# Kernel optimization log

Hardware: AMD Instinct MI355X
Metric: run time of the kernel (lower is better)

The kernel has to match this reference:

```python
import jax, jax.numpy as jnp
import numpy as np

D_MODEL = 2048
D_FF = 8192


def _act_quant(x):
    # BitNet b1.58 per-token int8 absmax activation quantization with STE passthrough
    scale = 127.0 / jnp.clip(jnp.max(jnp.abs(x), axis=-1, keepdims=True), 1e-5)
    xq = jnp.clip(jnp.round(x * scale), -128.0, 127.0) / scale
    return x + jax.lax.stop_gradient(xq - x)


def _weight_quant(w):
    # Ternary {-1,0,1} weight quantization with per-tensor mean-abs scale
    scale = 1.0 / jnp.clip(jnp.mean(jnp.abs(w)), 1e-5)
    wq = jnp.clip(jnp.round(w * scale), -1.0, 1.0) / scale
    return w + jax.lax.stop_gradient(wq - w)


def _bitlinear(x, w):
    # y = Q_act(x) @ Q_w(w)^T   (w has shape [out, in], torch Linear convention)
    return jnp.einsum('bsd,fd->bsf', _act_quant(x), _weight_quant(w))


def setup_inputs() -> dict:
    key = jax.random.key(0)
    k_x, k_w1, k_w2 = jax.random.split(key, 3)
    x = jax.random.normal(k_x, (4, 4096, D_MODEL), dtype=jnp.float32)
    # torch Linear default init scale ~ 1/sqrt(fan_in)
    W1 = jax.random.normal(k_w1, (D_FF, D_MODEL), dtype=jnp.float32) / np.sqrt(D_MODEL)
    W2 = jax.random.normal(k_w2, (D_MODEL, D_FF), dtype=jnp.float32) / np.sqrt(D_FF)
    return {"x": x, "W1": W1, "W2": W2}


def reference(x, W1, W2):
    h = jax.nn.silu(_bitlinear(x, W1))   # [B, S, d_ff]
    return _bitlinear(h, W2)             # [B, S, d_model]; dropout p=0 -> identity
```

## Files before the change

kernel.cpp:

```cpp
#include <hip/hip_runtime.h>
#include <hip/hip_bf16.h>
#include <cstdint>

#define DM 2048
#define DF 8192

typedef int v4i __attribute__((ext_vector_type(4)));

__device__ __forceinline__ float silu_f(float y) {
  return y * (1.0f / (1.0f + expf(-y)));
}

__device__ __forceinline__ void gload_lds16(const void* g, void* l) {
  __builtin_amdgcn_global_load_lds(
      (const __attribute__((address_space(1))) void*)g,
      (__attribute__((address_space(3))) void*)l, 16, 0, 0);
}

__global__ __launch_bounds__(256) void abs_sum_k(const float* __restrict__ w,
                                                 float* __restrict__ partial) {
  const int t = threadIdx.x;
  const float4* wp = (const float4*)w;
  const long base = (long)blockIdx.x * 4096;
  float s = 0.f;
#pragma unroll
  for (int i = 0; i < 16; ++i) {
    float4 v = wp[base + i * 256 + t];
    s += fabsf(v.x) + fabsf(v.y) + fabsf(v.z) + fabsf(v.w);
  }
#pragma unroll
  for (int d = 1; d < 64; d <<= 1) s += __shfl_xor(s, d, 64);
  __shared__ float wsum[4];
  if ((t & 63) == 0) wsum[t >> 6] = s;
  __syncthreads();
  if (t == 0) partial[blockIdx.x] = (wsum[0] + wsum[1]) + (wsum[2] + wsum[3]);
}

__global__ __launch_bounds__(256) void finalize_scales_k(const float* __restrict__ p1,
                                                         const float* __restrict__ p2,
                                                         float* __restrict__ sc) {
  const float* p = (blockIdx.x == 0) ? p1 : p2;
  const int t = threadIdx.x;
  float s = (p[t] + p[t + 256]) + (p[t + 512] + p[t + 768]);
#pragma unroll
  for (int d = 1; d < 64; d <<= 1) s += __shfl_xor(s, d, 64);
  __shared__ float wsum[4];
  if ((t & 63) == 0) wsum[t >> 6] = s;
  __syncthreads();
  if (t == 0) {
    float total = (wsum[0] + wsum[1]) + (wsum[2] + wsum[3]);
    float mean = total * (1.0f / 16777216.0f);
    float c = fmaxf(mean, 1e-5f);
    sc[blockIdx.x * 2 + 0] = 1.0f / c;
    sc[blockIdx.x * 2 + 1] = c;
  }
}

__global__ __launch_bounds__(256) void tern_quant_k(const float* __restrict__ w,
                                                    int8_t* __restrict__ wq,
                                                    const float* __restrict__ scp) {
  const float s = scp[0];
  const long i = (long)blockIdx.x * 256 + threadIdx.x;
  float4 v = ((const float4*)w)[i];
  int q0 = (int)rintf(v.x * s); q0 = q0 < -1 ? -1 : (q0 > 1 ? 1 : q0);
  int q1 = (int)rintf(v.y * s); q1 = q1 < -1 ? -1 : (q1 > 1 ? 1 : q1);
  int q2 = (int)rintf(v.z * s); q2 = q2 < -1 ? -1 : (q2 > 1 ? 1 : q2);
  int q3 = (int)rintf(v.w * s); q3 = q3 < -1 ? -1 : (q3 > 1 ? 1 : q3);
  ((int*)wq)[i] = (q0 & 255) | ((q1 & 255) << 8) | ((q2 & 255) << 16) | ((q3 & 255) << 24);
}

__global__ __launch_bounds__(256) void act_quant_x_k(const float* __restrict__ x,
                                                     int8_t* __restrict__ xq,
                                                     float* __restrict__ inv_sx) {
  const int t = threadIdx.x;
  const long row = blockIdx.x;
  const float4* xr = (const float4*)(x + row * DM);
  float4 v0 = xr[t * 2], v1 = xr[t * 2 + 1];
  float m = fmaxf(fmaxf(fmaxf(fabsf(v0.x), fabsf(v0.y)), fmaxf(fabsf(v0.z), fabsf(v0.w))),
                  fmaxf(fmaxf(fabsf(v1.x), fabsf(v1.y)), fmaxf(fabsf(v1.z), fabsf(v1.w))));
#pragma unroll
  for (int d = 1; d < 64; d <<= 1) m = fmaxf(m, __shfl_xor(m, d, 64));
  __shared__ float wm[4];
  if ((t & 63) == 0) wm[t >> 6] = m;
  __syncthreads();
  m = fmaxf(fmaxf(wm[0], wm[1]), fmaxf(wm[2], wm[3]));
  const float scale = 127.0f / fmaxf(m, 1e-5f);
  if (t == 0) inv_sx[row] = 1.0f / scale;
  float vv[8] = {v0.x, v0.y, v0.z, v0.w, v1.x, v1.y, v1.z, v1.w};
  int q[8];
#pragma unroll
  for (int j = 0; j < 8; ++j) {
    int qq = (int)rintf(vv[j] * scale);
    q[j] = qq < -128 ? -128 : (qq > 127 ? 127 : qq);
  }
  int lo = (q[0] & 255) | ((q[1] & 255) << 8) | ((q[2] & 255) << 16) | ((q[3] & 255) << 24);
  int hi = (q[4] & 255) | ((q[5] & 255) << 8) | ((q[6] & 255) << 16) | ((q[7] & 255) << 24);
  ((int2*)(xq + row * DM))[t] = make_int2(lo, hi);
}

template <int K, int N, int EPI>
__global__ __launch_bounds__(512, 2) void gemm8_i8_k(
    const int8_t* __restrict__ A, const int8_t* __restrict__ B,
    const float* __restrict__ rowInv, const float* __restrict__ invswp,
    short* __restrict__ Y16, float* __restrict__ rowmaxP,
    float* __restrict__ Out) {
  constexpr int NT = K / 128;
  constexpr int NBX = N / 256;
  __shared__ __align__(16) uint8_t lds[131072];

  const int t = threadIdx.x;
  const int wave = t >> 6;
  const int lane = t & 63;
  const int wr = wave >> 2;
  const int wc = wave & 3;
  const int l15 = lane & 15, l4 = lane >> 4;

  const int cpx = (int)gridDim.x >> 3;
  const int bid0 = blockIdx.x;
  const int bid = (bid0 & 7) * cpx + (bid0 >> 3);
  const int bx = bid % NBX, by = bid / NBX;
  const long arow0 = (long)by * 256;
  const long bcol0 = (long)bx * 256;

  const int8_t* Ablk = A + arow0 * K;
  const int8_t* Bblk = B + bcol0 * K;

  const int srow = t >> 3;
  const int scol = ((t & 7) ^ (srow & 7)) << 4;

  const int rAo = (wr * 128 + l15) * 128;
  const int rBo = (wc * 64 + l15) * 128;
  const int sw = (l15 & 7) << 4;
  const int cc0 = (l4 * 16) ^ sw;
  const int cc1 = (64 | (l4 * 16)) ^ sw;

  v4i acc[8][4] = {};
  v4i a[8][2], b[4][2];

#define STAGEHT(ht_)                                                             \
  do {                                                                           \
    const int ht = (ht_);                                                        \
    if (ht < 4 * NT) {                                                           \
      const int kts = ht >> 2, part = ht & 3;                                    \
      uint8_t* d0 = lds + ((kts & 1) << 16) + (part << 14) + (wave << 10);       \
      const int8_t* sp = (part < 2) ? Ablk : Bblk;                               \
      const int8_t* s0 =                                                         \
          sp + (long)(((part & 1) << 7) + srow) * K + ((long)kts << 7) + scol;   \
      gload_lds16(s0, d0);                                                       \
      gload_lds16(s0 + ((long)K << 6), d0 + 8192);                               \
    }                                                                            \
  } while (0)

#define BAR1()                                              \
  asm volatile("" ::: "memory");                            \
  __builtin_amdgcn_s_barrier();                             \
  asm volatile("s_waitcnt lgkmcnt(0)" ::: "memory")

#define BAR2()                                              \
  asm volatile("" ::: "memory");                            \
  __builtin_amdgcn_s_barrier()

#define MM(mi, ni)                                                                          \
  acc[mi][ni] = __builtin_amdgcn_mfma_i32_16x16x64_i8(a[mi][0], b[ni][0], acc[mi][ni], 0, 0, 0); \
  acc[mi][ni] = __builtin_amdgcn_mfma_i32_16x16x64_i8(a[mi][1], b[ni][1], acc[mi][ni], 0, 0, 0)

  STAGEHT(0); STAGEHT(1); STAGEHT(2); STAGEHT(3);
  STAGEHT(4); STAGEHT(5); STAGEHT(6);
  asm volatile("s_waitcnt vmcnt(6)" ::: "memory");
  __builtin_amdgcn_s_barrier();

  for (int kt = 0; kt < NT; ++kt) {
    const uint8_t* sA = lds + ((kt & 1) << 16);
    const uint8_t* sB = sA + 32768;

    #pragma unroll
    for (int mi = 0; mi < 4; ++mi) {
      a[mi][0] = *(const v4i*)(sA + rAo + mi * 2048 + cc0);
      a[mi][1] = *(const v4i*)(sA + rAo + mi * 2048 + cc1);
    }
    #pragma unroll
    for (int ni = 0; ni < 2; ++ni) {
      b[ni][0] = *(const v4i*)(sB + rBo + ni * 2048 + cc0);
      b[ni][1] = *(const v4i*)(sB + rBo + ni * 2048 + cc1);
    }
    STAGEHT(4 * kt + 7);
    BAR1();
    __builtin_amdgcn_s_setprio(1);
    MM(0, 0); MM(0, 1); MM(1, 0); MM(1, 1);
    MM(2, 0); MM(2, 1); MM(3, 0); MM(3, 1);
    __builtin_amdgcn_s_setprio(0);
    BAR2();

    #pragma unroll
    for (int mi = 4; mi < 8; ++mi) {
      a[mi][0] = *(const v4i*)(sA + rAo + mi * 2048 + cc0);
      a[mi][1] = *(const v4i*)(sA + rAo + mi * 2048 + cc1);
    }
    STAGEHT(4 * kt + 8);
    BAR1();
    __builtin_amdgcn_s_setprio(1);
    MM(4, 0); MM(4, 1); MM(5, 0); MM(5, 1);
    MM(6, 0); MM(6, 1); MM(7, 0); MM(7, 1);
    __builtin_amdgcn_s_setprio(0);
    BAR2();

    #pragma unroll
    for (int ni = 2; ni < 4; ++ni) {
      b[ni][0] = *(const v4i*)(sB + rBo + ni * 2048 + cc0);
      b[ni][1] = *(const v4i*)(sB + rBo + ni * 2048 + cc1);
    }
    STAGEHT(4 * kt + 9);
    BAR1();
    __builtin_amdgcn_s_setprio(1);
    MM(0, 2); MM(0, 3); MM(1, 2); MM(1, 3);
    MM(2, 2); MM(2, 3); MM(3, 2); MM(3, 3);
    __builtin_amdgcn_s_setprio(0);
    BAR2();

    STAGEHT(4 * kt + 10);
    BAR2();
    __builtin_amdgcn_s_setprio(1);
    MM(4, 2); MM(4, 3); MM(5, 2); MM(5, 3);
    MM(6, 2); MM(6, 3); MM(7, 2); MM(7, 3);
    __builtin_amdgcn_s_setprio(0);
    if (kt < NT - 2) {
      asm volatile("s_waitcnt vmcnt(6)" ::: "memory");
    } else if (kt == NT - 2) {
      asm volatile("s_waitcnt vmcnt(0)" ::: "memory");
    }
    BAR2();
  }

  const float invsw = invswp[0];
  if constexpr (EPI == 1) {
    __syncthreads();
    float* redmax = (float*)lds;
#pragma unroll
    for (int mi = 0; mi < 8; ++mi) {
#pragma unroll
      for (int r = 0; r < 4; ++r) {
        const int lrow = wr * 128 + mi * 16 + l4 * 4 + r;
        const long grow = arow0 + lrow;
        const float c1v = rowInv[grow] * invsw;
        float mx = 0.f;
#pragma unroll
        for (int ni = 0; ni < 4; ++ni) {
          int yi = acc[mi][ni][r];
          float h = silu_f((float)yi * c1v);
          mx = fmaxf(mx, fabsf(h));
          int ys = yi < -32767 ? -32767 : (yi > 32767 ? 32767 : yi);
          Y16[grow * (long)DF + bcol0 + wc * 64 + ni * 16 + l15] = (short)ys;
        }
#pragma unroll
        for (int d = 1; d < 16; d <<= 1) mx = fmaxf(mx, __shfl_xor(mx, d, 64));
        if (l15 == 0) redmax[lrow * 4 + wc] = mx;
      }
    }
    __syncthreads();
    if (t < 256) {
      float mm = fmaxf(fmaxf(redmax[t * 4], redmax[t * 4 + 1]),
                       fmaxf(redmax[t * 4 + 2], redmax[t * 4 + 3]));
      rowmaxP[(arow0 + t) * NBX + bx] = mm;
    }
  } else {
#pragma unroll
    for (int mi = 0; mi < 8; ++mi) {
#pragma unroll
      for (int r = 0; r < 4; ++r) {
        const long grow = arow0 + wr * 128 + mi * 16 + l4 * 4 + r;
        const float c2 = rowInv[grow] * invsw;
#pragma unroll
        for (int ni = 0; ni < 4; ++ni)
          Out[grow * N + bcol0 + wc * 64 + ni * 16 + l15] = (float)acc[mi][ni][r] * c2;
      }
    }
  }
#undef STAGEHT
#undef BAR1
#undef BAR2
#undef MM
}

__global__ __launch_bounds__(256) void quant_h_k(const short* __restrict__ Y16,
                                                 const float* __restrict__ rowmaxP,
                                                 const float* __restrict__ inv_sx,
                                                 const float* __restrict__ sc,
                                                 int8_t* __restrict__ hq,
                                                 float* __restrict__ inv_sh) {
  const int t = threadIdx.x;
  const long row = blockIdx.x;
  __shared__ float smax_s;
  if (t < 64) {
    float m = (t < 32) ? rowmaxP[row * 32 + t] : 0.f;
#pragma unroll
    for (int d = 1; d < 64; d <<= 1) m = fmaxf(m, __shfl_xor(m, d, 64));
    if (t == 0) smax_s = m;
  }
  __syncthreads();
  const float scale = 127.0f / fmaxf(smax_s, 1e-5f);
  if (t == 0) inv_sh[row] = 1.0f / scale;
  const float c1 = inv_sx[row] * sc[1];
  const short4* yp = (const short4*)(Y16 + row * DF);
  int* op = (int*)(hq + row * DF);
#pragma unroll
  for (int b = 0; b < 8; ++b) {
    short4 s4 = yp[b * 256 + t];
    short vals[4] = {s4.x, s4.y, s4.z, s4.w};
    int q[4];
#pragma unroll
    for (int j = 0; j < 4; ++j) {
      float h = silu_f((float)vals[j] * c1);
      int qq = (int)rintf(h * scale);
      q[j] = qq < -128 ? -128 : (qq > 127 ? 127 : qq);
    }
    op[b * 256 + t] = (q[0] & 255) | ((q[1] & 255) << 8) | ((q[2] & 255) << 16) | ((q[3] & 255) << 24);
  }
}

extern "C" void kernel_launch(void* const* d_in, const int* in_sizes, int n_in,
                              void* d_out, int out_size, void* d_ws, size_t ws_size,
                              hipStream_t stream) {
  const float* x = (const float*)d_in[0];
  const float* W1 = (const float*)d_in[1];
  const float* W2 = (const float*)d_in[2];
  float* out = (float*)d_out;

  uint8_t* w = (uint8_t*)d_ws;
  float* sc = (float*)(w + 0);
  float* p1 = (float*)(w + 256);
  float* p2 = (float*)(w + 256 + 4096);
  float* inv_sx = (float*)(w + 8448);
  float* inv_sh = (float*)(w + 8448 + 65536);
  float* rowmaxP = (float*)(w + 8448 + 131072);
  uint8_t* w1q = w + 8448 + 131072 + 4194304;
  uint8_t* w2q = w1q + 16777216;
  uint8_t* xq = w2q + 16777216;
  uint8_t* hq = xq + 33554432;
  short* y16 = (short*)(hq + 134217728);

  abs_sum_k<<<1024, 256, 0, stream>>>(W1, p1);
  abs_sum_k<<<1024, 256, 0, stream>>>(W2, p2);
  finalize_scales_k<<<2, 256, 0, stream>>>(p1, p2, sc);
  tern_quant_k<<<16384, 256, 0, stream>>>(W1, (int8_t*)w1q, sc + 0);
  tern_quant_k<<<16384, 256, 0, stream>>>(W2, (int8_t*)w2q, sc + 2);
  act_quant_x_k<<<16384, 256, 0, stream>>>(x, (int8_t*)xq, inv_sx);
  gemm8_i8_k<2048, 8192, 1><<<2048, 512, 0, stream>>>(
      (const int8_t*)xq, (const int8_t*)w1q, inv_sx, sc + 1, y16, rowmaxP, nullptr);
  quant_h_k<<<16384, 256, 0, stream>>>(y16, rowmaxP, inv_sx, sc, (int8_t*)hq, inv_sh);
  gemm8_i8_k<8192, 2048, 0><<<512, 512, 0, stream>>>(
      (const int8_t*)hq, (const int8_t*)w2q, inv_sh, sc + 3, nullptr, nullptr, out);
}
```

Measured before the change: 834.1 us.

## Restructure int8 GEMM main loop with fewer barriers and fragment-level pipelining

```diff
diff --git a/kernel.cpp b/kernel.cpp
--- a/kernel.cpp
+++ b/kernel.cpp
@@ -98,6 +98,21 @@
   ((int2*)(xq + row * DM))[t] = make_int2(lo, hi);
 }
 
+template <int MO, int NO>
+__device__ __forceinline__ void cluster(const v4i (&af)[4][2], const v4i (&bf)[2][2],
+                                        v4i (&acc)[8][4]) {
+  __builtin_amdgcn_s_setprio(1);
+#pragma unroll
+  for (int ks = 0; ks < 2; ++ks)
+#pragma unroll
+    for (int m = 0; m < 4; ++m)
+#pragma unroll
+      for (int n = 0; n < 2; ++n)
+        acc[MO + m][NO + n] = __builtin_amdgcn_mfma_i32_16x16x64_i8(
+            af[m][ks], bf[n][ks], acc[MO + m][NO + n], 0, 0, 0);
+  __builtin_amdgcn_s_setprio(0);
+}
+
 template <int K, int N, int EPI>
 __global__ __launch_bounds__(512, 2) void gemm8_i8_k(
     const int8_t* __restrict__ A, const int8_t* __restrict__ B,
@@ -135,100 +150,75 @@
   const int cc1 = (64 | (l4 * 16)) ^ sw;
 
   v4i acc[8][4] = {};
-  v4i a[8][2], b[4][2];
-
-#define STAGEHT(ht_)                                                             \
-  do {                                                                           \
-    const int ht = (ht_);                                                        \
-    if (ht < 4 * NT) {                                                           \
-      const int kts = ht >> 2, part = ht & 3;                                    \
-      uint8_t* d0 = lds + ((kts & 1) << 16) + (part << 14) + (wave << 10);       \
-      const int8_t* sp = (part < 2) ? Ablk : Bblk;                               \
-      const int8_t* s0 =                                                         \
-          sp + (long)(((part & 1) << 7) + srow) * K + ((long)kts << 7) + scol;   \
-      gload_lds16(s0, d0);                                                       \
-      gload_lds16(s0 + ((long)K << 6), d0 + 8192);                               \
-    }                                                                            \
+  v4i a_lo[4][2], a_hi[4][2], b_lo[2][2], b_hi[2][2];
+
+#define STAGE(ktile_, part_)                                                      \
+  do {                                                                            \
+    const int kk = (ktile_);                                                      \
+    if (kk < NT) {                                                                \
+      uint8_t* d0 = lds + ((kk & 1) << 16) + ((part_) << 14) + (wave << 10);      \
+      const int8_t* sp = ((part_) < 2) ? Ablk : Bblk;                             \
+      const int8_t* s0 =                                                          \
+          sp + (long)((((part_) & 1) << 7) + srow) * K + ((long)kk << 7) + scol;  \
+      gload_lds16(s0, d0);                                                        \
+      gload_lds16(s0 + ((long)K << 6), d0 + 8192);                                \
+    }                                                                             \
   } while (0)
 
-#define BAR1()                                              \
-  asm volatile("" ::: "memory");                            \
-  __builtin_amdgcn_s_barrier();                             \
-  asm volatile("s_waitcnt lgkmcnt(0)" ::: "memory")
-
-#define BAR2()                                              \
-  asm volatile("" ::: "memory");                            \
-  __builtin_amdgcn_s_barrier()
-
-#define MM(mi, ni)                                                                          \
-  acc[mi][ni] = __builtin_amdgcn_mfma_i32_16x16x64_i8(a[mi][0], b[ni][0], acc[mi][ni], 0, 0, 0); \
-  acc[mi][ni] = __builtin_amdgcn_mfma_i32_16x16x64_i8(a[mi][1], b[ni][1], acc[mi][ni], 0, 0, 0)
-
-  STAGEHT(0); STAGEHT(1); STAGEHT(2); STAGEHT(3);
-  STAGEHT(4); STAGEHT(5); STAGEHT(6);
-  asm volatile("s_waitcnt vmcnt(6)" ::: "memory");
+#define LGKM0 asm volatile("s_waitcnt lgkmcnt(0)" ::: "memory"); \
+              __builtin_amdgcn_sched_barrier(0)
+#define SB    __builtin_amdgcn_sched_barrier(0)
+
+  STAGE(0, 0); STAGE(0, 1); STAGE(0, 2); STAGE(0, 3);
+  STAGE(1, 0); STAGE(1, 1);
+  asm volatile("s_waitcnt vmcnt(4)" ::: "memory");
   __builtin_amdgcn_s_barrier();
 
   for (int kt = 0; kt < NT; ++kt) {
     const uint8_t* sA = lds + ((kt & 1) << 16);
     const uint8_t* sB = sA + 32768;
 
-    #pragma unroll
-    for (int mi = 0; mi < 4; ++mi) {
-      a[mi][0] = *(const v4i*)(sA + rAo + mi * 2048 + cc0);
-      a[mi][1] = *(const v4i*)(sA + rAo + mi * 2048 + cc1);
-    }
-    #pragma unroll
-    for (int ni = 0; ni < 2; ++ni) {
-      b[ni][0] = *(const v4i*)(sB + rBo + ni * 2048 + cc0);
-      b[ni][1] = *(const v4i*)(sB + rBo + ni * 2048 + cc1);
-    }
-    STAGEHT(4 * kt + 7);
-    BAR1();
-    __builtin_amdgcn_s_setprio(1);
-    MM(0, 0); MM(0, 1); MM(1, 0); MM(1, 1);
-    MM(2, 0); MM(2, 1); MM(3, 0); MM(3, 1);
-    __builtin_amdgcn_s_setprio(0);
-    BAR2();
-
-    #pragma unroll
-    for (int mi = 4; mi < 8; ++mi) {
-      a[mi][0] = *(const v4i*)(sA + rAo + mi * 2048 + cc0);
-      a[mi][1] = *(const v4i*)(sA + rAo + mi * 2048 + cc1);
-    }
-    STAGEHT(4 * kt + 8);
-    BAR1();
-    __builtin_amdgcn_s_setprio(1);
-    MM(4, 0); MM(4, 1); MM(5, 0); MM(5, 1);
-    MM(6, 0); MM(6, 1); MM(7, 0); MM(7, 1);
-    __builtin_amdgcn_s_setprio(0);
-    BAR2();
-
-    #pragma unroll
-    for (int ni = 2; ni < 4; ++ni) {
-      b[ni][0] = *(const v4i*)(sB + rBo + ni * 2048 + cc0);
-      b[ni][1] = *(const v4i*)(sB + rBo + ni * 2048 + cc1);
-    }
-    STAGEHT(4 * kt + 9);
-    BAR1();
-    __builtin_amdgcn_s_setprio(1);
-    MM(0, 2); MM(0, 3); MM(1, 2); MM(1, 3);
-    MM(2, 2); MM(2, 3); MM(3, 2); MM(3, 3);
-    __builtin_amdgcn_s_setprio(0);
-    BAR2();
-
-    STAGEHT(4 * kt + 10);
-    BAR2();
-    __builtin_amdgcn_s_setprio(1);
-    MM(4, 2); MM(4, 3); MM(5, 2); MM(5, 3);
-    MM(6, 2); MM(6, 3); MM(7, 2); MM(7, 3);
-    __builtin_amdgcn_s_setprio(0);
+#pragma unroll
+    for (int m = 0; m < 4; ++m) {
+      a_lo[m][0] = *(const v4i*)(sA + rAo + m * 2048 + cc0);
+      a_lo[m][1] = *(const v4i*)(sA + rAo + m * 2048 + cc1);
+    }
+#pragma unroll
+    for (int n = 0; n < 2; ++n) {
+      b_lo[n][0] = *(const v4i*)(sB + rBo + n * 2048 + cc0);
+      b_lo[n][1] = *(const v4i*)(sB + rBo + n * 2048 + cc1);
+    }
+    STAGE(kt + 1, 2);
+    LGKM0;
+#pragma unroll
+    for (int m = 0; m < 4; ++m) {
+      a_hi[m][0] = *(const v4i*)(sA + rAo + (m + 4) * 2048 + cc0);
+      a_hi[m][1] = *(const v4i*)(sA + rAo + (m + 4) * 2048 + cc1);
+    }
+    STAGE(kt + 1, 3);
+    SB;
+    cluster<0, 0>(a_lo, b_lo, acc);
+    LGKM0;
+#pragma unroll
+    for (int n = 0; n < 2; ++n) {
+      b_hi[n][0] = *(const v4i*)(sB + rBo + (n + 2) * 2048 + cc0);
+      b_hi[n][1] = *(const v4i*)(sB + rBo + (n + 2) * 2048 + cc1);
+    }
+    __builtin_amdgcn_s_barrier();
+    STAGE(kt + 2, 0);
+    SB;
+    cluster<4, 0>(a_hi, b_lo, acc);
+    LGKM0;
+    STAGE(kt + 2, 1);
+    SB;
+    cluster<0, 2>(a_lo, b_hi, acc);
+    cluster<4, 2>(a_hi, b_hi, acc);
     if (kt < NT - 2) {
-      asm volatile("s_waitcnt vmcnt(6)" ::: "memory");
+      asm volatile("s_waitcnt vmcnt(4)" ::: "memory");
     } else if (kt == NT - 2) {
       asm volatile("s_waitcnt vmcnt(0)" ::: "memory");
     }
-    BAR2();
+    __builtin_amdgcn_s_barrier();
   }
 
   const float invsw = invswp[0];
@@ -275,10 +265,9 @@
       }
     }
   }
-#undef STAGEHT
-#undef BAR1
-#undef BAR2
-#undef MM
+#undef STAGE
+#undef LGKM0
+#undef SB
 }
 
 __global__ __launch_bounds__(256) void quant_h_k(const short* __restrict__ Y16,
```

Result: no change. 820.5 us (-1.6%).
